# Kernel optimization log

Hardware: AMD Instinct MI355X
Metric: run time of the kernel (lower is better)

## Reference

```python
import jax, jax.numpy as jnp
import numpy as np

D_MODEL = 1024
D_STATE = 16
D_CONV = 4
EXPAND = 2
D_INNER = EXPAND * D_MODEL  # 2048
DT_RANK = (D_MODEL + 15) // 16  # 64
BATCH, SEQLEN = 2, 2048


def setup_inputs() -> dict:
    key = jax.random.key(0)
    ks = jax.random.split(key, 10)
    sc = 0.02
    # dt bias init as in the torch module: inv_softplus of dt ~ LogUniform(1e-3, 0.1)
    dt = jnp.exp(jax.random.uniform(ks[6], (D_INNER,), minval=np.log(1e-3), maxval=np.log(0.1)))
    dt_proj_b = jnp.log(jnp.expm1(dt))
    A_log = jnp.log(jnp.broadcast_to(jnp.arange(1, D_STATE + 1, dtype=jnp.float32), (D_INNER, D_STATE)))
    return {
        "hidden_states": jax.random.normal(ks[0], (BATCH, SEQLEN, D_MODEL), jnp.float32),
        "in_proj_w": jax.random.normal(ks[1], (2 * D_INNER, D_MODEL), jnp.float32) * sc,
        "conv_w": jax.random.normal(ks[2], (D_INNER, D_CONV), jnp.float32) * sc,
        "conv_b": jax.random.normal(ks[3], (D_INNER,), jnp.float32) * sc,
        "x_proj_w": jax.random.normal(ks[4], (DT_RANK + 2 * D_STATE, D_INNER), jnp.float32) * sc,
        "dt_proj_w": jax.random.normal(ks[5], (D_INNER, DT_RANK), jnp.float32) * (DT_RANK ** -0.5),
        "dt_proj_b": dt_proj_b,
        "A_log": A_log,
        "D": jnp.ones((D_INNER,), jnp.float32),
        "out_proj_w": jax.random.normal(ks[7], (D_MODEL, D_INNER), jnp.float32) * sc,
    }


def reference(hidden_states, in_proj_w, conv_w, conv_b, x_proj_w, dt_proj_w, dt_proj_b, A_log, D, out_proj_w):
    b, l, d_model = hidden_states.shape
    d_inner = conv_w.shape[0]
    n = A_log.shape[1]
    # input projection -> (b, l, 2*d_inner), split into x and gate z
    xz = jnp.einsum('bld,ed->ble', hidden_states, in_proj_w)
    x, z = jnp.split(xz, 2, axis=-1)
    # causal depthwise conv over L, then SiLU
    x_cl = jnp.transpose(x, (0, 2, 1))  # (b, d_inner, l)
    x_conv = jax.lax.conv_general_dilated(
        x_cl, conv_w[:, None, :],  # (O=d_inner, I=1, W)
        window_strides=(1,), padding=[(D_CONV - 1, 0)],
        dimension_numbers=('NCH', 'OIH', 'NCH'),
        feature_group_count=d_inner)
    x_conv = jax.nn.silu(x_conv + conv_b[None, :, None])  # (b, d_inner, l)
    # data-dependent SSM params
    x_dbl = jnp.einsum('bdl,ed->ble', x_conv, x_proj_w)  # (b, l, dt_rank + 2n)
    dt_r, Bm, Cm = jnp.split(x_dbl, [DT_RANK, DT_RANK + n], axis=-1)
    delta = jax.nn.softplus(jnp.einsum('blr,dr->bld', dt_r, dt_proj_w) + dt_proj_b)  # (b, l, d_inner)
    A = -jnp.exp(A_log)  # (d_inner, n)
    # selective scan over sequence (sequential recurrence via lax.scan)
    u = jnp.transpose(x_conv, (2, 0, 1))      # (l, b, d_inner)
    dlt = jnp.transpose(delta, (1, 0, 2))     # (l, b, d_inner)
    Bl = jnp.transpose(Bm, (1, 0, 2))         # (l, b, n)
    Cl = jnp.transpose(Cm, (1, 0, 2))         # (l, b, n)

    def step(state, inputs):
        u_t, d_t, B_t, C_t = inputs  # (b,d), (b,d), (b,n), (b,n)
        dA = jnp.exp(d_t[:, :, None] * A[None])                # (b, d, n)
        dBu = (d_t * u_t)[:, :, None] * B_t[:, None, :]        # (b, d, n)
        state = state * dA + dBu
        y_t = jnp.einsum('bdn,bn->bd', state, C_t) + D * u_t
        return state, y_t

    init = jnp.zeros((b, d_inner, n), jnp.float32)
    _, ys = jax.lax.scan(step, init, (u, dlt, Bl, Cl))
    y = jnp.transpose(ys, (1, 0, 2))  # (b, l, d_inner)
    y = y * jax.nn.silu(z)
    out = jnp.einsum('bld,od->blo', y, out_proj_w)
    return out
```

## Files before the change

kernel.cpp:

```cpp
#include <hip/hip_runtime.h>
#include <hip/hip_bf16.h>
#include <cstdint>
#include <cstddef>

#define D_MODEL 1024
#define D_STATE 16
#define D_INNER 2048
#define DT_RANK 64
#define BATCH 2
#define SEQLEN 2048
#define BL (BATCH*SEQLEN)
#define NPROJ 96
#define NCHUNK 64
#define CLEN 32
#define G2_KSLICE 8
#define G2_KLEN (D_INNER / G2_KSLICE)

static_assert(NCHUNK * CLEN == SEQLEN, "chunking");
static_assert((size_t)D_STATE * BATCH * NCHUNK * D_INNER == (size_t)BL * D_MODEL,
              "init aliases d_out exactly");
static_assert((size_t)G2_KSLICE * BL * 128 * 4 ==
              (size_t)BL * D_MODEL * 2 + (size_t)2 * D_INNER * D_MODEL * 2,
              "Cpart alias fits exactly");

typedef __hip_bfloat16 bf16;
using f32x4 = __attribute__((ext_vector_type(4))) float;
using s16x8 = __attribute__((ext_vector_type(8))) short;

__device__ __forceinline__ unsigned short f2bf(float f) {
  union { float f; unsigned int u; } v; v.f = f;
  unsigned int r = v.u + 0x7fffu + ((v.u >> 16) & 1u);
  return (unsigned short)(r >> 16);
}

__device__ __forceinline__ float bf2f(unsigned short u) {
  return __uint_as_float(((unsigned int)u) << 16);
}

__device__ __forceinline__ void async16(const void* g, void* l) {
  __builtin_amdgcn_global_load_lds(
      (const __attribute__((address_space(1))) void*)g,
      (__attribute__((address_space(3))) void*)l,
      16, 0, 0);
}

__device__ __forceinline__ void cvt4(const float* __restrict__ in,
                                     bf16* __restrict__ out, int i) {
  const float4 v = *reinterpret_cast<const float4*>(&in[(size_t)i * 4]);
  ushort4 o;
  o.x = f2bf(v.x); o.y = f2bf(v.y); o.z = f2bf(v.z); o.w = f2bf(v.w);
  *reinterpret_cast<ushort4*>(&out[(size_t)i * 4]) = o;
}

#define CAST_NH  (BL * D_MODEL / 4)
#define CAST_NW1 (2 * D_INNER * D_MODEL / 4)
#define CAST_NW4 (D_MODEL * D_INNER / 4)
#define CAST_NWP (128 * D_INNER / 4)
#define CAST_TOTAL (CAST_NH + CAST_NW1 + CAST_NW4 + CAST_NWP)
static_assert(CAST_TOTAL % 256 == 0, "cast grid");

__global__ __launch_bounds__(256) void cast_all(
    const float* __restrict__ hidden, const float* __restrict__ w1,
    const float* __restrict__ w4, const float* __restrict__ xpw,
    bf16* __restrict__ hbf, bf16* __restrict__ w1bf,
    bf16* __restrict__ w4bf, bf16* __restrict__ wpad)
{
  const int i = blockIdx.x * 256 + threadIdx.x;
  if (i < CAST_NH) {
    cvt4(hidden, hbf, i);
  } else if (i < CAST_NH + CAST_NW1) {
    cvt4(w1, w1bf, i - CAST_NH);
  } else if (i < CAST_NH + CAST_NW1 + CAST_NW4) {
    cvt4(w4, w4bf, i - CAST_NH - CAST_NW1);
  } else {
    const int j = i - CAST_NH - CAST_NW1 - CAST_NW4;
    const int n = j >> 9;
    const int k4 = j & 511;
    ushort4 o = {0, 0, 0, 0};
    if (n < NPROJ) {
      const float4 v = *reinterpret_cast<const float4*>(&xpw[(size_t)n * D_INNER + k4 * 4]);
      o.x = f2bf(v.x); o.y = f2bf(v.y); o.z = f2bf(v.z); o.w = f2bf(v.w);
    }
    *reinterpret_cast<ushort4*>(&wpad[(size_t)n * D_INNER + k4 * 4]) = o;
  }
}

__global__ __launch_bounds__(512, 2) void gemm1_256(
    const bf16* __restrict__ A, const bf16* __restrict__ B,
    float* __restrict__ C0, float* __restrict__ C1,
    int M, int N, int K, int N0)
{
  extern __shared__ char smem[];
  const int tid  = threadIdx.x;
  const int lane = tid & 63;
  const int wid  = tid >> 6;
  const int wr   = wid >> 2;
  const int wc   = wid & 3;
  const int m0 = blockIdx.y * 256;
  const int n0 = blockIdx.x * 256;
  const int lrow = lane & 15;
  const int kg   = lane >> 4;
  const int sr4  = lane >> 2;
  const int sg   = lane & 3;
  const int NT = K >> 6;

  f32x4 acc[8][4] = {};

  auto stage = [&](int t, int db) {
    const int kb = t * 64;
#pragma unroll
    for (int j = 0; j < 4; ++j) {
      const int ia = wid * 4 + j;
      const int s = ia >> 4;
      const int r = (ia & 15) * 16 + sr4;
      const int gs = sg ^ ((r >> 2) & 3);
      async16(A + (size_t)(m0 + r) * K + kb + s * 32 + gs * 8,
              smem + db * 32768 + ia * 1024);
      async16(B + (size_t)(n0 + r) * K + kb + s * 32 + gs * 8,
              smem + 65536 + db * 32768 + ia * 1024);
    }
  };

  auto compute = [&](int db) {
    const char* ab = smem + db * 32768;
    const char* bb = ab + 65536;
    s16x8 bfr[4][2];
#pragma unroll
    for (int nf = 0; nf < 4; ++nf) {
      const int r = wc * 64 + nf * 16 + lrow;
      const int gsw = kg ^ ((r >> 2) & 3);
#pragma unroll
      for (int s = 0; s < 2; ++s)
        bfr[nf][s] = *reinterpret_cast<const s16x8*>(bb + s * 16384 + r * 64 + gsw * 16);
    }
#pragma unroll
    for (int mf = 0; mf < 8; ++mf) {
      const int r = wr * 128 + mf * 16 + lrow;
      const int gsw = kg ^ ((r >> 2) & 3);
      const s16x8 a0 = *reinterpret_cast<const s16x8*>(ab + r * 64 + gsw * 16);
      const s16x8 a1 = *reinterpret_cast<const s16x8*>(ab + 16384 + r * 64 + gsw * 16);
#pragma unroll
      for (int nf = 0; nf < 4; ++nf) {
        acc[mf][nf] = __builtin_amdgcn_mfma_f32_16x16x32_bf16(a0, bfr[nf][0], acc[mf][nf], 0, 0, 0);
        acc[mf][nf] = __builtin_amdgcn_mfma_f32_16x16x32_bf16(a1, bfr[nf][1], acc[mf][nf], 0, 0, 0);
      }
    }
  };

  stage(0, 0);
  __syncthreads();
  for (int t = 0; t < NT; ++t) {
    const int db = t & 1;
    if (t + 1 < NT) stage(t + 1, db ^ 1);
    compute(db);
    __syncthreads();
  }

  const int N1 = N - N0;
  const bool inC0 = (n0 < N0);
  float* Cb = inC0 ? C0 : C1;
  const int stride = inC0 ? N0 : N1;
  const int cb = inC0 ? n0 : (n0 - N0);
#pragma unroll
  for (int mf = 0; mf < 8; ++mf) {
    const int row0 = m0 + wr * 128 + mf * 16 + kg * 4;
#pragma unroll
    for (int nf = 0; nf < 4; ++nf) {
      const int col = cb + wc * 64 + nf * 16 + lrow;
      const f32x4 v = acc[mf][nf];
      float* p = Cb + (size_t)row0 * stride + col;
#pragma unroll
      for (int r = 0; r < 4; ++r) p[(size_t)r * stride] = v[r];
    }
  }
}

__global__ __launch_bounds__(256, 2) void gemm_out_128x64(
    const bf16* __restrict__ A, const bf16* __restrict__ B,
    float* __restrict__ C, int M, int N, int K)
{
  extern __shared__ char smem[];
  const int tid  = threadIdx.x;
  const int lane = tid & 63;
  const int wid  = tid >> 6;
  const int wr   = wid >> 1;
  const int wc   = wid & 1;
  const int m0 = blockIdx.y * 128;
  const int n0 = blockIdx.x * 64;
  const int lrow = lane & 15;
  const int kg   = lane >> 4;
  const int sr4  = lane >> 2;
  const int sg   = lane & 3;
  const int NT = K >> 6;

  f32x4 acc[4][2] = {};

  auto stage = [&](int t, int db) {
    const int kb = t * 64;
#pragma unroll
    for (int j = 0; j < 4; ++j) {
      const int ia = wid * 4 + j;
      const int s = ia >> 3;
      const int r = (ia & 7) * 16 + sr4;
      const int gs = sg ^ ((r >> 2) & 3);
      async16(A + (size_t)(m0 + r) * K + kb + s * 32 + gs * 8,
              smem + db * 16384 + ia * 1024);
    }
#pragma unroll
    for (int j = 0; j < 2; ++j) {
      const int ib = wid * 2 + j;
      const int s = ib >> 2;
      const int r = (ib & 3) * 16 + sr4;
      const int gs = sg ^ ((r >> 2) & 3);
      async16(B + (size_t)(n0 + r) * K + kb + s * 32 + gs * 8,
              smem + 32768 + db * 8192 + ib * 1024);
    }
  };

  auto compute = [&](int db) {
    const char* ab = smem + db * 16384;
    const char* bb = smem + 32768 + db * 8192;
    s16x8 bfr[2][2];
#pragma unroll
    for (int nf = 0; nf < 2; ++nf) {
      const int r = wc * 32 + nf * 16 + lrow;
      const int gsw = kg ^ ((r >> 2) & 3);
      bfr[nf][0] = *reinterpret_cast<const s16x8*>(bb + r * 64 + gsw * 16);
      bfr[nf][1] = *reinterpret_cast<const s16x8*>(bb + 4096 + r * 64 + gsw * 16);
    }
#pragma unroll
    for (int mf = 0; mf < 4; ++mf) {
      const int r = wr * 64 + mf * 16 + lrow;
      const int gsw = kg ^ ((r >> 2) & 3);
      const s16x8 a0 = *reinterpret_cast<const s16x8*>(ab + r * 64 + gsw * 16);
      const s16x8 a1 = *reinterpret_cast<const s16x8*>(ab + 8192 + r * 64 + gsw * 16);
#pragma unroll
      for (int nf = 0; nf < 2; ++nf) {
        acc[mf][nf] = __builtin_amdgcn_mfma_f32_16x16x32_bf16(a0, bfr[nf][0], acc[mf][nf], 0, 0, 0);
        acc[mf][nf] = __builtin_amdgcn_mfma_f32_16x16x32_bf16(a1, bfr[nf][1], acc[mf][nf], 0, 0, 0);
      }
    }
  };

  stage(0, 0);
  __syncthreads();
  for (int t = 0; t < NT; ++t) {
    const int db = t & 1;
    if (t + 1 < NT) stage(t + 1, db ^ 1);
    compute(db);
    __syncthreads();
  }

#pragma unroll
  for (int mf = 0; mf < 4; ++mf) {
    const int row0 = m0 + wr * 64 + mf * 16 + kg * 4;
#pragma unroll
    for (int nf = 0; nf < 2; ++nf) {
      const int col = n0 + wc * 32 + nf * 16 + lrow;
      const f32x4 v = acc[mf][nf];
      float* p = C + (size_t)row0 * N + col;
#pragma unroll
      for (int r = 0; r < 4; ++r) p[(size_t)r * N] = v[r];
    }
  }
}

__global__ __launch_bounds__(256) void gemm2_mfma(
    const bf16* __restrict__ A, const bf16* __restrict__ B,
    float* __restrict__ Cpart)
{
  __shared__ __align__(16) bf16 As[128 * 32];
  __shared__ __align__(16) bf16 Bs[128 * 32];
  const int tid  = threadIdx.x;
  const int lane = tid & 63;
  const int wave = tid >> 6;
  const int wr = wave >> 1, wc = wave & 1;
  const int kz = blockIdx.x, by = blockIdx.y;

  const int srow = lane >> 2;
  const int scol = (lane & 3) * 8;
  const int c0 = wave * 2, c1 = wave * 2 + 1;
  const int kbase = kz * G2_KLEN;
  const bf16* gA0 = A + (size_t)(by * 128 + c0 * 16 + srow) * D_INNER + kbase + scol;
  const bf16* gA1 = A + (size_t)(by * 128 + c1 * 16 + srow) * D_INNER + kbase + scol;
  const bf16* gB0 = B + (size_t)(c0 * 16 + srow) * D_INNER + kbase + scol;
  const bf16* gB1 = B + (size_t)(c1 * 16 + srow) * D_INNER + kbase + scol;
  bf16* lA0 = &As[c0 * 512];
  bf16* lA1 = &As[c1 * 512];
  bf16* lB0 = &Bs[c0 * 512];
  bf16* lB1 = &Bs[c1 * 512];

  f32x4 acc[4][4] = {};
  const int lrow = lane & 15;
  const int lkb  = (lane >> 4) * 8;

  for (int ks = 0; ks < G2_KLEN; ks += 32) {
    async16(gA0 + ks, lA0);
    async16(gA1 + ks, lA1);
    async16(gB0 + ks, lB0);
    async16(gB1 + ks, lB1);
    __syncthreads();
    s16x8 af[4], bfr[4];
#pragma unroll
    for (int i = 0; i < 4; ++i) {
      af[i]  = *reinterpret_cast<const s16x8*>(&As[(wr * 64 + i * 16 + lrow) * 32 + lkb]);
      bfr[i] = *reinterpret_cast<const s16x8*>(&Bs[(wc * 64 + i * 16 + lrow) * 32 + lkb]);
    }
#pragma unroll
    for (int i = 0; i < 4; ++i)
#pragma unroll
      for (int j = 0; j < 4; ++j)
        acc[i][j] = __builtin_amdgcn_mfma_f32_16x16x32_bf16(af[i], bfr[j], acc[i][j], 0, 0, 0);
    __syncthreads();
  }

  float* Cz = Cpart + (size_t)kz * BL * 128;
#pragma unroll
  for (int i = 0; i < 4; ++i) {
    const int row0 = by * 128 + wr * 64 + i * 16 + (lane >> 4) * 4;
#pragma unroll
    for (int j = 0; j < 4; ++j) {
      const int col = wc * 64 + j * 16 + (lane & 15);
      const f32x4 v = acc[i][j];
      float* p = Cz + (size_t)row0 * 128 + col;
#pragma unroll
      for (int r = 0; r < 4; ++r) p[(size_t)r * 128] = v[r];
    }
  }
}

__global__ __launch_bounds__(256) void reduce_xdbl(
    const float* __restrict__ Cpart, float* __restrict__ xdbl)
{
  const int i = blockIdx.x * 256 + threadIdx.x;
  const int m = i / 24;
  const int g = i - m * 24;
  f32x4 s = {};
#pragma unroll
  for (int z = 0; z < G2_KSLICE; ++z)
    s += *reinterpret_cast<const f32x4*>(&Cpart[((size_t)z * BL + m) * 128 + g * 4]);
  *reinterpret_cast<f32x4*>(&xdbl[(size_t)m * NPROJ + g * 4]) = s;
}

__global__ __launch_bounds__(256) void conv_silu_k(
    const float* __restrict__ x, const float* __restrict__ cw,
    const float* __restrict__ cb, bf16* __restrict__ ubf)
{
  const int idx = blockIdx.x * 256 + threadIdx.x;
  const int d  = idx & (D_INNER - 1);
  const int bl = idx >> 11;
  const int l  = bl & (SEQLEN - 1);
  const float4 w = *reinterpret_cast<const float4*>(&cw[d * 4]);
  const float* xp = x + (size_t)bl * D_INNER + d;
  float acc = cb[d] + w.w * xp[0];
  if (l >= 1) acc += w.z * xp[-D_INNER];
  if (l >= 2) acc += w.y * xp[-2 * D_INNER];
  if (l >= 3) acc += w.x * xp[-3 * D_INNER];
  const float val = acc / (1.f + __expf(-acc));
  reinterpret_cast<unsigned short*>(ubf)[idx] = f2bf(val);
}

__device__ __forceinline__ float softplusf(float x) {
  return (x > 20.f) ? x : log1pf(__expf(x));
}

__global__ __launch_bounds__(256) void gemm3_delta(
    const float* __restrict__ xdbl, const float* __restrict__ Wdt,
    const float* __restrict__ bdt, float* __restrict__ delta)
{
  __shared__ __align__(16) float aT[64][132];
  __shared__ __align__(16) float bT[64][68];
  const int t = threadIdx.x;
  const int n0 = blockIdx.x * 64;
  const int m0 = blockIdx.y * 128;

  {
    const int r  = t & 127;
    const int k0 = (t >> 7) * 32;
    const float* src = xdbl + (size_t)(m0 + r) * NPROJ + k0;
#pragma unroll
    for (int p = 0; p < 8; ++p) {
      const float4 v = *reinterpret_cast<const float4*>(&src[p * 4]);
      aT[k0 + p * 4 + 0][r] = v.x;
      aT[k0 + p * 4 + 1][r] = v.y;
      aT[k0 + p * 4 + 2][r] = v.z;
      aT[k0 + p * 4 + 3][r] = v.w;
    }
  }
  {
    const int r  = t & 63;
    const int k0 = (t >> 6) * 16;
    const float* src = Wdt + (size_t)(n0 + r) * DT_RANK + k0;
#pragma unroll
    for (int p = 0; p < 4; ++p) {
      const float4 v = *reinterpret_cast<const float4*>(&src[p * 4]);
      bT[k0 + p * 4 + 0][r] = v.x;
      bT[k0 + p * 4 + 1][r] = v.y;
      bT[k0 + p * 4 + 2][r] = v.z;
      bT[k0 + p * 4 + 3][r] = v.w;
    }
  }
  __syncthreads();

  const int tx = t & 15;
  const int ty = t >> 4;
  f32x4 acc[8] = {};
#pragma unroll 4
  for (int kk = 0; kk < 64; ++kk) {
    const f32x4 a0 = *reinterpret_cast<const f32x4*>(&aT[kk][ty * 8]);
    const f32x4 a1 = *reinterpret_cast<const f32x4*>(&aT[kk][ty * 8 + 4]);
    const f32x4 b  = *reinterpret_cast<const f32x4*>(&bT[kk][tx * 4]);
    acc[0] += a0.x * b;  acc[1] += a0.y * b;
    acc[2] += a0.z * b;  acc[3] += a0.w * b;
    acc[4] += a1.x * b;  acc[5] += a1.y * b;
    acc[6] += a1.z * b;  acc[7] += a1.w * b;
  }

  const float4 bias = *reinterpret_cast<const float4*>(&bdt[n0 + tx * 4]);
#pragma unroll
  for (int i = 0; i < 8; ++i) {
    const int m = m0 + ty * 8 + i;
    float4 o;
    o.x = softplusf(acc[i].x + bias.x);
    o.y = softplusf(acc[i].y + bias.y);
    o.z = softplusf(acc[i].z + bias.z);
    o.w = softplusf(acc[i].w + bias.w);
    *reinterpret_cast<float4*>(&delta[(size_t)m * D_INNER + n0 + tx * 4]) = o;
  }
}

__global__ __launch_bounds__(256) void scan_p1(
    const float* __restrict__ delta, const bf16* __restrict__ ubf,
    const float* __restrict__ xdbl, const float* __restrict__ A_log,
    float* __restrict__ P, float* __restrict__ S)
{
  const int t = threadIdx.x;
  const int d = ((blockIdx.x & 7) << 8) + t;
  const int c = (blockIdx.x >> 3) & (NCHUNK - 1);
  const int b = blockIdx.x >> 9;

  float a[D_STATE];
  {
    const f32x4* ap = reinterpret_cast<const f32x4*>(&A_log[d * D_STATE]);
#pragma unroll
    for (int q = 0; q < 4; ++q) {
      const f32x4 v = ap[q];
      a[4 * q + 0] = -__expf(v.x); a[4 * q + 1] = -__expf(v.y);
      a[4 * q + 2] = -__expf(v.z); a[4 * q + 3] = -__expf(v.w);
    }
  }

  float s[D_STATE] = {};
  float sumdl = 0.f;

  const size_t rbase = (size_t)(b * SEQLEN + c * CLEN);
  const float* dp = delta + rbase * D_INNER + d;
  const unsigned short* up = reinterpret_cast<const unsigned short*>(ubf) + rbase * D_INNER + d;
  const float* xr = xdbl  + rbase * NPROJ + DT_RANK;

  for (int l = 0; l < CLEN; ++l) {
    const float dl = dp[(size_t)l * D_INNER];
    const float ul = bf2f(up[(size_t)l * D_INNER]);
    const float du = dl * ul;
    sumdl += dl;
    const float* Brow = xr + (size_t)l * NPROJ;
#pragma unroll
    for (int n = 0; n < D_STATE; ++n)
      s[n] = s[n] * __expf(dl * a[n]) + du * Brow[n];
  }

  const size_t plane = (size_t)BATCH * NCHUNK * D_INNER;
  const size_t pbase = ((size_t)b * NCHUNK + c) * D_INNER + d;
#pragma unroll
  for (int n = 0; n < D_STATE; ++n) {
    P[n * plane + pbase] = __expf(sumdl * a[n]);
    S[n * plane + pbase] = s[n];
  }
}

__global__ __launch_bounds__(256) void scan_p2(
    const float* __restrict__ P, const float* __restrict__ S,
    float* __restrict__ init)
{
  const int gid = blockIdx.x * 256 + threadIdx.x;
  const int d  = gid & (D_INNER - 1);
  const int nb = gid >> 11;

  float carry = 0.f;
#pragma unroll 8
  for (int c = 0; c < NCHUNK; ++c) {
    const size_t o = ((size_t)nb * NCHUNK + c) * D_INNER + d;
    init[o] = carry;
    carry = carry * P[o] + S[o];
  }
}

__global__ __launch_bounds__(256) void scan_p3(
    const float* __restrict__ delta, const bf16* __restrict__ ubf,
    const float* __restrict__ z, const float* __restrict__ xdbl,
    const float* __restrict__ A_log, const float* __restrict__ Dvec,
    const float* __restrict__ init, bf16* __restrict__ y)
{
  const int t = threadIdx.x;
  const int d = ((blockIdx.x & 7) << 8) + t;
  const int c = (blockIdx.x >> 3) & (NCHUNK - 1);
  const int b = blockIdx.x >> 9;

  float a[D_STATE];
  {
    const f32x4* ap = reinterpret_cast<const f32x4*>(&A_log[d * D_STATE]);
#pragma unroll
    for (int q = 0; q < 4; ++q) {
      const f32x4 v = ap[q];
      a[4 * q + 0] = -__expf(v.x); a[4 * q + 1] = -__expf(v.y);
      a[4 * q + 2] = -__expf(v.z); a[4 * q + 3] = -__expf(v.w);
    }
  }
  const float Dd = Dvec[d];

  const size_t plane = (size_t)BATCH * NCHUNK * D_INNER;
  const size_t pbase = ((size_t)b * NCHUNK + c) * D_INNER + d;
  float s[D_STATE];
#pragma unroll
  for (int n = 0; n < D_STATE; ++n)
    s[n] = init[n * plane + pbase];

  const size_t rbase = (size_t)(b * SEQLEN + c * CLEN);
  const float* dp = delta + rbase * D_INNER + d;
  const unsigned short* up = reinterpret_cast<const unsigned short*>(ubf) + rbase * D_INNER + d;
  const float* zp = z     + rbase * D_INNER + d;
  const float* xr = xdbl  + rbase * NPROJ + DT_RANK;
  unsigned short* yp = reinterpret_cast<unsigned short*>(y) + rbase * D_INNER + d;

  for (int l = 0; l < CLEN; ++l) {
    const float dl = dp[(size_t)l * D_INNER];
    const float ul = bf2f(up[(size_t)l * D_INNER]);
    const float zl = zp[(size_t)l * D_INNER];
    const float du = dl * ul;
    const float* Brow = xr + (size_t)l * NPROJ;
    float y0 = 0.f, y1 = 0.f, y2 = 0.f, y3 = 0.f;
#pragma unroll
    for (int q = 0; q < 4; ++q) {
      float p0 = 0.f;
#pragma unroll
      for (int j = 0; j < 4; ++j) {
        const int n = q * 4 + j;
        s[n] = s[n] * __expf(dl * a[n]) + du * Brow[n];
        p0 += s[n] * Brow[D_STATE + n];
      }
      if (q == 0) y0 = p0; else if (q == 1) y1 = p0;
      else if (q == 2) y2 = p0; else y3 = p0;
    }
    const float yv = ((y0 + y1) + (y2 + y3) + Dd * ul) * (zl / (1.f + __expf(-zl)));
    yp[(size_t)l * D_INNER] = f2bf(yv);
  }
}

extern "C" void kernel_launch(void* const* d_in, const int* in_sizes, int n_in,
                              void* d_out, int out_size, void* d_ws, size_t ws_size,
                              hipStream_t stream)
{
  (void)in_sizes; (void)n_in; (void)out_size; (void)ws_size;
  const float* hidden    = (const float*)d_in[0];
  const float* in_projw  = (const float*)d_in[1];
  const float* conv_w    = (const float*)d_in[2];
  const float* conv_b    = (const float*)d_in[3];
  const float* x_projw   = (const float*)d_in[4];
  const float* dt_projw  = (const float*)d_in[5];
  const float* dt_projb  = (const float*)d_in[6];
  const float* A_log     = (const float*)d_in[7];
  const float* Dvec      = (const float*)d_in[8];
  const float* out_projw = (const float*)d_in[9];
  float* out = (float*)d_out;

  char* ws = (char*)d_ws;
  size_t off = 0;
  auto alloc = [&](size_t bytes) -> void* {
    void* p = ws + off;
    off += (bytes + 255) & ~(size_t)255;
    return p;
  };
  float* x    = (float*)alloc((size_t)BL * D_INNER * 4);
  float* zbuf = (float*)alloc((size_t)BL * D_INNER * 4);
  float* dbuf = (float*)alloc((size_t)BL * D_INNER * 4);
  float* xdbl = (float*)alloc((size_t)BL * NPROJ * 4);
  bf16* hbf   = (bf16*)alloc((size_t)BL * D_MODEL * 2);
  bf16* w1bf  = (bf16*)alloc((size_t)2 * D_INNER * D_MODEL * 2);
  bf16* w4bf  = (bf16*)alloc((size_t)D_MODEL * D_INNER * 2);
  float* Sbuf = (float*)alloc((size_t)D_STATE * BATCH * NCHUNK * D_INNER * 4);
  bf16* ubf   = (bf16*)alloc((size_t)BL * D_INNER * 2);
  bf16* wpad  = (bf16*)alloc((size_t)128 * D_INNER * 2);
  bf16* ybf   = (bf16*)x;
  float* Cpart = (float*)hbf;
  float* Pbuf  = (float*)hbf;
  float* init  = out;

  cast_all<<<CAST_TOTAL / 256, 256, 0, stream>>>(
      hidden, in_projw, out_projw, x_projw, hbf, w1bf, w4bf, wpad);

  hipFuncSetAttribute(reinterpret_cast<const void*>(gemm1_256),
                      hipFuncAttributeMaxDynamicSharedMemorySize, 131072);
  gemm1_256<<<dim3((2 * D_INNER) / 256, BL / 256), 512, 131072, stream>>>(
      hbf, w1bf, x, zbuf, BL, 2 * D_INNER, D_MODEL, D_INNER);

  conv_silu_k<<<BL * D_INNER / 256, 256, 0, stream>>>(x, conv_w, conv_b, ubf);

  gemm2_mfma<<<dim3(G2_KSLICE, BL / 128), 256, 0, stream>>>(ubf, wpad, Cpart);
  reduce_xdbl<<<BL * 24 / 256, 256, 0, stream>>>(Cpart, xdbl);

  gemm3_delta<<<dim3(D_INNER / 64, BL / 128), 256, 0, stream>>>(xdbl, dt_projw, dt_projb, dbuf);

  const int nblk = BATCH * NCHUNK * (D_INNER / 256);
  scan_p1<<<nblk, 256, 0, stream>>>(dbuf, ubf, xdbl, A_log, Pbuf, Sbuf);
  scan_p2<<<(BATCH * D_INNER * D_STATE) / 256, 256, 0, stream>>>(Pbuf, Sbuf, init);
  scan_p3<<<nblk, 256, 0, stream>>>(dbuf, ubf, zbuf, xdbl, A_log, Dvec, init, ybf);

  hipFuncSetAttribute(reinterpret_cast<const void*>(gemm_out_128x64),
                      hipFuncAttributeMaxDynamicSharedMemorySize, 49152);
  gemm_out_128x64<<<dim3(D_MODEL / 64, BL / 128), 256, 49152, stream>>>(
      ybf, w4bf, out, BL, D_MODEL, D_INNER);
}
```

Measured before the change: 252.6 us.

## Move dt projection GEMM to bf16 MFMA with async LDS loads

Replaces the fp32 FMA-based dt_proj GEMM with a bf16 MFMA kernel on 128x128 tiles. The dt-rank slice of x_dbl is cast to bf16 in the reduce kernel, and dt_proj weights are cast in the cast pass. Operands are staged into swizzled LDS with global_load_lds before the MFMA loop. The intent is to cut the compute time of this K=64 GEMM, at the cost of bf16 rounding in the delta input and output stores that only coalesce across 16 columns.

New measurement: 239.0 us. 5.4% less time.

```diff
diff --git a/kernel.cpp b/kernel.cpp
--- a/kernel.cpp
+++ b/kernel.cpp
@@ -56,14 +56,17 @@
 #define CAST_NW1 (2 * D_INNER * D_MODEL / 4)
 #define CAST_NW4 (D_MODEL * D_INNER / 4)
 #define CAST_NWP (128 * D_INNER / 4)
-#define CAST_TOTAL (CAST_NH + CAST_NW1 + CAST_NW4 + CAST_NWP)
+#define CAST_NDT (D_INNER * DT_RANK / 4)
+#define CAST_TOTAL (CAST_NH + CAST_NW1 + CAST_NW4 + CAST_NWP + CAST_NDT)
 static_assert(CAST_TOTAL % 256 == 0, "cast grid");
 
 __global__ __launch_bounds__(256) void cast_all(
     const float* __restrict__ hidden, const float* __restrict__ w1,
     const float* __restrict__ w4, const float* __restrict__ xpw,
+    const float* __restrict__ wdt,
     bf16* __restrict__ hbf, bf16* __restrict__ w1bf,
-    bf16* __restrict__ w4bf, bf16* __restrict__ wpad)
+    bf16* __restrict__ w4bf, bf16* __restrict__ wpad,
+    bf16* __restrict__ wdtbf)
 {
   const int i = blockIdx.x * 256 + threadIdx.x;
   if (i < CAST_NH) {
@@ -72,7 +75,7 @@
     cvt4(w1, w1bf, i - CAST_NH);
   } else if (i < CAST_NH + CAST_NW1 + CAST_NW4) {
     cvt4(w4, w4bf, i - CAST_NH - CAST_NW1);
-  } else {
+  } else if (i < CAST_NH + CAST_NW1 + CAST_NW4 + CAST_NWP) {
     const int j = i - CAST_NH - CAST_NW1 - CAST_NW4;
     const int n = j >> 9;
     const int k4 = j & 511;
@@ -82,6 +85,8 @@
       o.x = f2bf(v.x); o.y = f2bf(v.y); o.z = f2bf(v.z); o.w = f2bf(v.w);
     }
     *reinterpret_cast<ushort4*>(&wpad[(size_t)n * D_INNER + k4 * 4]) = o;
+  } else {
+    cvt4(wdt, wdtbf, i - CAST_NH - CAST_NW1 - CAST_NW4 - CAST_NWP);
   }
 }
 
@@ -330,7 +335,8 @@
 }
 
 __global__ __launch_bounds__(256) void reduce_xdbl(
-    const float* __restrict__ Cpart, float* __restrict__ xdbl)
+    const float* __restrict__ Cpart, float* __restrict__ xdbl,
+    bf16* __restrict__ dtrbf)
 {
   const int i = blockIdx.x * 256 + threadIdx.x;
   const int m = i / 24;
@@ -340,6 +346,11 @@
   for (int z = 0; z < G2_KSLICE; ++z)
     s += *reinterpret_cast<const f32x4*>(&Cpart[((size_t)z * BL + m) * 128 + g * 4]);
   *reinterpret_cast<f32x4*>(&xdbl[(size_t)m * NPROJ + g * 4]) = s;
+  if (g < 16) {
+    ushort4 o;
+    o.x = f2bf(s[0]); o.y = f2bf(s[1]); o.z = f2bf(s[2]); o.w = f2bf(s[3]);
+    *reinterpret_cast<ushort4*>(&dtrbf[(size_t)m * DT_RANK + g * 4]) = o;
+  }
 }
 
 __global__ __launch_bounds__(256) void conv_silu_k(
@@ -364,68 +375,74 @@
   return (x > 20.f) ? x : log1pf(__expf(x));
 }
 
-__global__ __launch_bounds__(256) void gemm3_delta(
-    const float* __restrict__ xdbl, const float* __restrict__ Wdt,
+__global__ __launch_bounds__(256) void gemm3_mfma(
+    const bf16* __restrict__ A, const bf16* __restrict__ B,
     const float* __restrict__ bdt, float* __restrict__ delta)
 {
-  __shared__ __align__(16) float aT[64][132];
-  __shared__ __align__(16) float bT[64][68];
-  const int t = threadIdx.x;
-  const int n0 = blockIdx.x * 64;
+  __shared__ __align__(16) char smem[32768];
+  const int tid  = threadIdx.x;
+  const int lane = tid & 63;
+  const int wid  = tid >> 6;
+  const int wr   = wid >> 1;
+  const int wc   = wid & 1;
+  const int n0 = blockIdx.x * 128;
   const int m0 = blockIdx.y * 128;
-
-  {
-    const int r  = t & 127;
-    const int k0 = (t >> 7) * 32;
-    const float* src = xdbl + (size_t)(m0 + r) * NPROJ + k0;
-#pragma unroll
-    for (int p = 0; p < 8; ++p) {
-      const float4 v = *reinterpret_cast<const float4*>(&src[p * 4]);
-      aT[k0 + p * 4 + 0][r] = v.x;
-      aT[k0 + p * 4 + 1][r] = v.y;
-      aT[k0 + p * 4 + 2][r] = v.z;
-      aT[k0 + p * 4 + 3][r] = v.w;
-    }
-  }
-  {
-    const int r  = t & 63;
-    const int k0 = (t >> 6) * 16;
-    const float* src = Wdt + (size_t)(n0 + r) * DT_RANK + k0;
-#pragma unroll
-    for (int p = 0; p < 4; ++p) {
-      const float4 v = *reinterpret_cast<const float4*>(&src[p * 4]);
-      bT[k0 + p * 4 + 0][r] = v.x;
-      bT[k0 + p * 4 + 1][r] = v.y;
-      bT[k0 + p * 4 + 2][r] = v.z;
-      bT[k0 + p * 4 + 3][r] = v.w;
-    }
+  const int lrow = lane & 15;
+  const int kg   = lane >> 4;
+  const int sr4  = lane >> 2;
+  const int sg   = lane & 3;
+
+#pragma unroll
+  for (int j = 0; j < 4; ++j) {
+    const int ia = wid * 4 + j;
+    const int s = ia >> 3;
+    const int r = (ia & 7) * 16 + sr4;
+    const int gs = sg ^ ((r >> 2) & 3);
+    async16(A + (size_t)(m0 + r) * DT_RANK + s * 32 + gs * 8,
+            smem + ia * 1024);
+    async16(B + (size_t)(n0 + r) * DT_RANK + s * 32 + gs * 8,
+            smem + 16384 + ia * 1024);
   }
   __syncthreads();
 
-  const int tx = t & 15;
-  const int ty = t >> 4;
-  f32x4 acc[8] = {};
-#pragma unroll 4
-  for (int kk = 0; kk < 64; ++kk) {
-    const f32x4 a0 = *reinterpret_cast<const f32x4*>(&aT[kk][ty * 8]);
-    const f32x4 a1 = *reinterpret_cast<const f32x4*>(&aT[kk][ty * 8 + 4]);
-    const f32x4 b  = *reinterpret_cast<const f32x4*>(&bT[kk][tx * 4]);
-    acc[0] += a0.x * b;  acc[1] += a0.y * b;
-    acc[2] += a0.z * b;  acc[3] += a0.w * b;
-    acc[4] += a1.x * b;  acc[5] += a1.y * b;
-    acc[6] += a1.z * b;  acc[7] += a1.w * b;
-  }
-
-  const float4 bias = *reinterpret_cast<const float4*>(&bdt[n0 + tx * 4]);
-#pragma unroll
-  for (int i = 0; i < 8; ++i) {
-    const int m = m0 + ty * 8 + i;
-    float4 o;
-    o.x = softplusf(acc[i].x + bias.x);
-    o.y = softplusf(acc[i].y + bias.y);
-    o.z = softplusf(acc[i].z + bias.z);
-    o.w = softplusf(acc[i].w + bias.w);
-    *reinterpret_cast<float4*>(&delta[(size_t)m * D_INNER + n0 + tx * 4]) = o;
+  f32x4 acc[4][4] = {};
+  const char* ab = smem;
+  const char* bb = smem + 16384;
+  s16x8 bfr[4][2];
+#pragma unroll
+  for (int nf = 0; nf < 4; ++nf) {
+    const int r = wc * 64 + nf * 16 + lrow;
+    const int gsw = kg ^ ((r >> 2) & 3);
+    bfr[nf][0] = *reinterpret_cast<const s16x8*>(bb + r * 64 + gsw * 16);
+    bfr[nf][1] = *reinterpret_cast<const s16x8*>(bb + 8192 + r * 64 + gsw * 16);
+  }
+#pragma unroll
+  for (int mf = 0; mf < 4; ++mf) {
+    const int r = wr * 64 + mf * 16 + lrow;
+    const int gsw = kg ^ ((r >> 2) & 3);
+    const s16x8 a0 = *reinterpret_cast<const s16x8*>(ab + r * 64 + gsw * 16);
+    const s16x8 a1 = *reinterpret_cast<const s16x8*>(ab + 8192 + r * 64 + gsw * 16);
+#pragma unroll
+    for (int nf = 0; nf < 4; ++nf) {
+      acc[mf][nf] = __builtin_amdgcn_mfma_f32_16x16x32_bf16(a0, bfr[nf][0], acc[mf][nf], 0, 0, 0);
+      acc[mf][nf] = __builtin_amdgcn_mfma_f32_16x16x32_bf16(a1, bfr[nf][1], acc[mf][nf], 0, 0, 0);
+    }
+  }
+
+#pragma unroll
+  for (int nf = 0; nf < 4; ++nf) {
+    const int col = n0 + wc * 64 + nf * 16 + lrow;
+    const float bias = bdt[col];
+#pragma unroll
+    for (int mf = 0; mf < 4; ++mf) {
+      const int row0 = m0 + wr * 64 + mf * 16 + kg * 4;
+      const f32x4 v = acc[mf][nf];
+      float* p = delta + (size_t)row0 * D_INNER + col;
+      p[0]                    = softplusf(v[0] + bias);
+      p[D_INNER]              = softplusf(v[1] + bias);
+      p[2 * (size_t)D_INNER]  = softplusf(v[2] + bias);
+      p[3 * (size_t)D_INNER]  = softplusf(v[3] + bias);
+    }
   }
 }
 
@@ -590,13 +607,16 @@
   float* Sbuf = (float*)alloc((size_t)D_STATE * BATCH * NCHUNK * D_INNER * 4);
   bf16* ubf   = (bf16*)alloc((size_t)BL * D_INNER * 2);
   bf16* wpad  = (bf16*)alloc((size_t)128 * D_INNER * 2);
+  bf16* wdtbf = (bf16*)alloc((size_t)D_INNER * DT_RANK * 2);
+  bf16* dtrbf = (bf16*)alloc((size_t)BL * DT_RANK * 2);
   bf16* ybf   = (bf16*)x;
   float* Cpart = (float*)hbf;
   float* Pbuf  = (float*)hbf;
   float* init  = out;
 
   cast_all<<<CAST_TOTAL / 256, 256, 0, stream>>>(
-      hidden, in_projw, out_projw, x_projw, hbf, w1bf, w4bf, wpad);
+      hidden, in_projw, out_projw, x_projw, dt_projw,
+      hbf, w1bf, w4bf, wpad, wdtbf);
 
   hipFuncSetAttribute(reinterpret_cast<const void*>(gemm1_256),
                       hipFuncAttributeMaxDynamicSharedMemorySize, 131072);
@@ -606,9 +626,10 @@
   conv_silu_k<<<BL * D_INNER / 256, 256, 0, stream>>>(x, conv_w, conv_b, ubf);
 
   gemm2_mfma<<<dim3(G2_KSLICE, BL / 128), 256, 0, stream>>>(ubf, wpad, Cpart);
-  reduce_xdbl<<<BL * 24 / 256, 256, 0, stream>>>(Cpart, xdbl);
-
-  gemm3_delta<<<dim3(D_INNER / 64, BL / 128), 256, 0, stream>>>(xdbl, dt_projw, dt_projb, dbuf);
+  reduce_xdbl<<<BL * 24 / 256, 256, 0, stream>>>(Cpart, xdbl, dtrbf);
+
+  gemm3_mfma<<<dim3(D_INNER / 128, BL / 128), 256, 0, stream>>>(
+      dtrbf, wdtbf, dt_projb, dbuf);
 
   const int nblk = BATCH * NCHUNK * (D_INNER / 256);
   scan_p1<<<nblk, 256, 0, stream>>>(dbuf, ubf, xdbl, A_log, Pbuf, Sbuf);
```
